# Performance work log

Measured on AMD Instinct MI355X. Metric: run time of the kernel, lower is better.

## Reference

```python
import jax, jax.numpy as jnp
import numpy as np
from jax import lax

BS, NV, CTX = 16, 7, 1536
PLEN, STRIDE = 16, 8
PN = (CTX - PLEN) // STRIDE + 1 + 1  # 192: end replication-pad adds one patch
D, H, DFF, L, TW = 512, 8, 2048, 3, 336
DK = D // H
SCALE = DK ** -0.5  # lsa=False -> fixed scale
NF = D * PN


def setup_inputs() -> dict:
    key = jax.random.key(0)
    ks = iter(jax.random.split(key, 40))

    def p(*shape, s=0.02):
        return jax.random.normal(next(ks), shape, jnp.float32) * s

    z = jax.random.normal(next(ks), (BS, NV, CTX), jnp.float32)
    # simpowerlaw decay mask: -|t|^scale, causal (-inf for k>q), one copy per layer
    t = np.arange(PN)
    times = t[:, None] - t[None, :]
    m = -np.abs(times).astype(np.float32) ** 0.25
    m[times < 0] = -np.inf
    decay_mask = jnp.asarray(np.broadcast_to(m, (L, PN, PN)).copy())
    return dict(
        z=z,
        W_P=p(PLEN, D), b_P=jnp.zeros((D,), jnp.float32),
        W_pos=p(PN, D),
        Wq=p(L, D, D), bq=jnp.zeros((L, D), jnp.float32),
        Wk=p(L, D, D), bk=jnp.zeros((L, D), jnp.float32),
        Wv=p(L, D, D), bv=jnp.zeros((L, D), jnp.float32),
        Wo=p(L, D, D), bo=jnp.zeros((L, D), jnp.float32),
        ln1_g=jnp.ones((L, D), jnp.float32), ln1_b=jnp.zeros((L, D), jnp.float32),
        W1=p(L, D, DFF), b1=jnp.zeros((L, DFF), jnp.float32),
        W2=p(L, DFF, D), b2=jnp.zeros((L, D), jnp.float32),
        ln2_g=jnp.ones((L, D), jnp.float32), ln2_b=jnp.zeros((L, D), jnp.float32),
        W_head=p(NF, TW, s=0.005), b_head=jnp.zeros((TW,), jnp.float32),
        decay_mask=decay_mask,
    )


def _ln(x, g, b):
    mu = x.mean(-1, keepdims=True)
    var = ((x - mu) ** 2).mean(-1, keepdims=True)
    return g * (x - mu) * lax.rsqrt(var + 1e-5) + b


def _forward(z, W_P, b_P, W_pos, Wq, bq, Wk, bk, Wv, bv, Wo, bo,
             ln1_g, ln1_b, W1, b1, W2, b2, ln2_g, ln2_b, W_head, b_head, decay_mask):
    bs, nv, _ = z.shape
    # replication pad end by STRIDE, then unfold into patches
    zp = jnp.concatenate([z, jnp.repeat(z[..., -1:], STRIDE, axis=-1)], axis=-1)
    idx = jnp.arange(PN)[:, None] * STRIDE + jnp.arange(PLEN)[None, :]
    patches = zp[..., idx]                      # [bs,nv,PN,PLEN]
    x = patches @ W_P + b_P                     # [bs,nv,PN,D]
    B = bs * nv
    src = x.reshape(B, PN, D) + W_pos           # channel-independent batch
    prev = jnp.zeros((B, H, PN, PN), src.dtype)  # residual attention carry

    def layer(carry, p):
        s, pr = carry
        wq, bq_, wk, bk_, wv, bv_, wo, bo_, g1, e1, w1, c1, w2, c2, g2, e2, dm = p
        q = (s @ wq + bq_).reshape(B, PN, H, DK).transpose(0, 2, 1, 3)
        k = (s @ wk + bk_).reshape(B, PN, H, DK).transpose(0, 2, 1, 3)
        v = (s @ wv + bv_).reshape(B, PN, H, DK).transpose(0, 2, 1, 3)
        scores = jnp.einsum('bhqd,bhkd->bhqk', q, k) * SCALE + pr + dm
        attn = jax.nn.softmax(scores, axis=-1)
        o = jnp.einsum('bhqk,bhkd->bhqd', attn, v).transpose(0, 2, 1, 3).reshape(B, PN, D)
        o = o @ wo + bo_
        s = _ln(s + o, g1, e1)                  # post-norm
        ff = jax.nn.gelu(s @ w1 + c1, approximate=False) @ w2 + c2
        s = _ln(s + ff, g2, e2)
        return (s, scores), None

    (src, _), _ = lax.scan(
        layer, (src, prev),
        (Wq, bq, Wk, bk, Wv, bv, Wo, bo, ln1_g, ln1_b, W1, b1, W2, b2, ln2_g, ln2_b, decay_mask))

    # Flatten_Head (individual=False): [bs,nv,D,PN] -> [bs,nv,D*PN] -> target_window
    xo = src.reshape(bs, nv, PN, D).transpose(0, 1, 3, 2).reshape(bs, nv, NF)
    return xo @ W_head + b_head                 # [bs,nv,TW]


def reference(z, W_P, b_P, W_pos, Wq, bq, Wk, bk, Wv, bv, Wo, bo,
              ln1_g, ln1_b, W1, b1, W2, b2, ln2_g, ln2_b, W_head, b_head, decay_mask):
    return _forward(z, W_P, b_P, W_pos, Wq, bq, Wk, bk, Wv, bv, Wo, bo,
                    ln1_g, ln1_b, W1, b1, W2, b2, ln2_g, ln2_b, W_head, b_head, decay_mask)
```

## Files before the change

kernel.cpp:

```cpp
#include <hip/hip_runtime.h>
#include <math.h>

#define BSZ 16
#define NV 7
#define CTX 1536
#define PN 192
#define PLEN 16
#define STRIDE 8
#define D 512
#define H 8
#define DK 64
#define DFF 2048
#define LYR 3
#define TW 336
#define NB 112
#define RTOT (NB * PN)
#define NF (D * PN)
#define SCALE 0.125f

typedef __attribute__((ext_vector_type(8))) short s16x8;
typedef __attribute__((ext_vector_type(4))) short s16x4;
typedef __attribute__((ext_vector_type(4))) float f32x4;

__device__ __forceinline__ unsigned short f2b(float f) {
  unsigned u = __builtin_bit_cast(unsigned, f);
  u = u + 0x7fffu + ((u >> 16) & 1u);
  return (unsigned short)(u >> 16);
}
__device__ __forceinline__ float b2f(unsigned short h) {
  unsigned u = ((unsigned)h) << 16;
  return __builtin_bit_cast(float, u);
}
__device__ __forceinline__ unsigned cvtpk(float lo, float hi) {
  unsigned r;
  asm("v_cvt_pk_bf16_f32 %0, %1, %2" : "=v"(r) : "v"(lo), "v"(hi));
  return r;
}
__device__ __forceinline__ float fast_exp2(float x) {
  float r; asm("v_exp_f32 %0, %1" : "=v"(r) : "v"(x)); return r;
}
__device__ __forceinline__ float fast_rcp(float x) {
  float r; asm("v_rcp_f32 %0, %1" : "=v"(r) : "v"(x)); return r;
}

__device__ __forceinline__ void glld(const unsigned short* g, short* l) {
  __builtin_amdgcn_global_load_lds(
      (const __attribute__((address_space(1))) void*)g,
      (__attribute__((address_space(3))) void*)l, 16, 0, 0);
}

__device__ __forceinline__ float gelu(float x) {
  float x2 = x * x;
  float u2 = x * fmaf(0.1029492f, x2, 2.3021186f);
  u2 = fminf(fmaxf(u2, -60.f), 60.f);
  float w = fast_exp2(u2);
  return x * w * fast_rcp(w + 1.0f);
}

__global__ __launch_bounds__(256) void k_patch_embed(
    const float* __restrict__ z, const float* __restrict__ W_P,
    const float* __restrict__ b_P, const float* __restrict__ W_pos,
    unsigned short* __restrict__ s) {
  int r = blockIdx.x;
  int bi = r / PN, p = r % PN;
  __shared__ float pv[PLEN];
  if (threadIdx.x < PLEN) {
    int t = p * STRIDE + threadIdx.x;
    pv[threadIdx.x] = z[(size_t)bi * CTX + (t < CTX ? t : CTX - 1)];
  }
  __syncthreads();
  for (int c = threadIdx.x; c < D; c += 256) {
    float acc = b_P[c] + W_pos[p * D + c];
#pragma unroll
    for (int j = 0; j < PLEN; j++) acc += pv[j] * W_P[j * D + c];
    s[(size_t)r * D + c] = f2b(acc);
  }
}

__global__ __launch_bounds__(256) void k_wtz(
    const float* __restrict__ W, unsigned short* __restrict__ Wt, int K, int N,
    size_t sstride, size_t dstride) {
  __shared__ float tile[32][33];
  const float* Wz = W + (size_t)blockIdx.z * sstride;
  unsigned short* Wtz = Wt + (size_t)blockIdx.z * dstride;
  int n0 = blockIdx.x * 32, k0 = blockIdx.y * 32;
  int tx = threadIdx.x & 31, ty = threadIdx.x >> 5;
#pragma unroll
  for (int i = 0; i < 4; i++)
    tile[ty + 8 * i][tx] =
        (n0 + tx < N) ? Wz[(size_t)(k0 + ty + 8 * i) * N + n0 + tx] : 0.0f;
  __syncthreads();
#pragma unroll
  for (int i = 0; i < 4; i++)
    if (n0 + ty + 8 * i < N)
      Wtz[(size_t)(n0 + ty + 8 * i) * K + k0 + tx] = f2b(tile[tx][ty + 8 * i]);
}

enum { EPI_QKV = 0, EPI_RES = 1, EPI_GELU = 2 };

template <int EPI, int N, int K>
__global__ __launch_bounds__(256) void k_mgemm(
    const unsigned short* __restrict__ Ap, const unsigned short* __restrict__ Wt,
    const float* __restrict__ bias0, const float* __restrict__ bias1,
    const float* __restrict__ bias2, const unsigned short* __restrict__ res,
    unsigned short* __restrict__ out0, unsigned short* __restrict__ out1,
    unsigned short* __restrict__ out2) {
  __shared__ short smem[24576];
  constexpr int NSTEP = K / 32;
  const int nx = N >> 7;
  const int nwg = gridDim.x;
  const int orig = blockIdx.x;
  const int wgid = (orig & 7) * (nwg >> 3) + (orig >> 3);
  const int m0 = (wgid / nx) * 128, n0 = (wgid % nx) * 128;
  const int t = threadIdx.x;
  const int w = t >> 6, l = t & 63;
  const int wr = (w >> 1) * 64, wc = (w & 1) * 64;
  const int lr = l & 15, lq = l >> 4;
  const int rsw = ((lr >> 1) & 3) << 3;
  const int srow = w * 32 + (l >> 2);
  const int scol = 8 * ((l & 3) ^ ((l >> 3) & 3));
  const unsigned short* gA = Ap + (size_t)(m0 + srow) * K + scol;
  const unsigned short* gB = Wt + (size_t)(n0 + srow) * K + scol;
  const int sbo = (w * 32) * 32;
  f32x4 acc[4][4] = {};

  auto STAGE = [&](int b, int kt) {
    short* dA = &smem[b * 8192 + sbo];
    short* dB = &smem[b * 8192 + 4096 + sbo];
    const int k0 = kt * 32;
    glld(gA + k0, dA);
    glld(gA + k0 + (size_t)16 * K, dA + 512);
    glld(gB + k0, dB);
    glld(gB + k0 + (size_t)16 * K, dB + 512);
  };

  STAGE(0, 0);
  STAGE(1, 1);
  int bc = 0, bs = 2;
  for (int step = 0; step < NSTEP; step++) {
    if (step + 2 < NSTEP) STAGE(bs, step + 2);
    if (step + 2 < NSTEP)      asm volatile("s_waitcnt vmcnt(8)" ::: "memory");
    else if (step + 1 < NSTEP) asm volatile("s_waitcnt vmcnt(4)" ::: "memory");
    else                       asm volatile("s_waitcnt vmcnt(0)" ::: "memory");
    __builtin_amdgcn_s_barrier();
    const short* cA = &smem[bc * 8192];
    const short* cB = &smem[bc * 8192 + 4096];
    s16x8 af[4], bf[4];
#pragma unroll
    for (int i = 0; i < 4; i++)
      af[i] = *(const s16x8*)&cA[(wr + i * 16 + lr) * 32 + ((lq * 8) ^ rsw)];
#pragma unroll
    for (int i = 0; i < 4; i++)
      bf[i] = *(const s16x8*)&cB[(wc + i * 16 + lr) * 32 + ((lq * 8) ^ rsw)];
#pragma unroll
    for (int i = 0; i < 4; i++)
#pragma unroll
      for (int j2 = 0; j2 < 4; j2++)
        acc[i][j2] = __builtin_amdgcn_mfma_f32_16x16x32_bf16(bf[j2], af[i], acc[i][j2], 0, 0, 0);
    asm volatile("s_waitcnt lgkmcnt(0)" ::: "memory");
    __builtin_amdgcn_s_barrier();
    bc++; if (bc == 3) bc = 0;
    bs++; if (bs == 3) bs = 0;
  }

  short* ot = smem;
  if (EPI == EPI_QKV) {
    const int which = n0 >> 9;
    const int ccb = n0 & 511;
    const float* bias = (which == 0) ? bias0 : (which == 1) ? bias1 : bias2;
    unsigned short* dst = (which == 0) ? out0 : (which == 1) ? out1 : out2;
    if (which < 2) {
#pragma unroll
      for (int i = 0; i < 4; i++) {
        const int ml = wr + i * 16 + lr;
#pragma unroll
        for (int j2 = 0; j2 < 4; j2++) {
          const int nl = wc + j2 * 16 + lq * 4;
          f32x4 a = acc[i][j2];
          float4 b4 = *(const float4*)&bias[ccb + nl];
          unsigned lo = cvtpk(a[0] + b4.x, a[1] + b4.y);
          unsigned hi = cvtpk(a[2] + b4.z, a[3] + b4.w);
          unsigned* d = (unsigned*)&ot[ml * 128 + ((nl >> 3) ^ (ml & 15)) * 8 + (nl & 7)];
          d[0] = lo; d[1] = hi;
        }
      }
      __syncthreads();
      const int r0 = t >> 1, cb = (t & 1) * 8;
      const int m = m0 + r0;
      const int bi2 = m / PN, p = m % PN;
#pragma unroll
      for (int q = 0; q < 8; q++) {
        int c = cb + q;
        int cc = ccb + c * 8;
        int hh = cc >> 6, dk8 = cc & 63;
        s16x8 vv = *(const s16x8*)&ot[r0 * 128 + ((c ^ (r0 & 15)) * 8)];
        *(s16x8*)&dst[(((size_t)bi2 * H + hh) * PN + p) * DK + dk8] = vv;
      }
    } else {
#pragma unroll
      for (int i = 0; i < 4; i++) {
        const int m = m0 + wr + i * 16 + lr;
        const int bi2 = m / PN, p = m % PN;
#pragma unroll
        for (int j2 = 0; j2 < 4; j2++) {
          const int nl = wc + j2 * 16 + lq * 4;
          f32x4 a = acc[i][j2];
#pragma unroll
          for (int r = 0; r < 4; r++) {
            int cc = ccb + nl + r;
            int hh = cc >> 6, dkk = cc & 63;
            dst[(((size_t)bi2 * H + hh) * DK + dkk) * PN + p] = f2b(a[r] + bias[cc]);
          }
        }
      }
    }
  } else {
#pragma unroll
    for (int i = 0; i < 4; i++) {
      const int ml = wr + i * 16 + lr;
#pragma unroll
      for (int j2 = 0; j2 < 4; j2++) {
        const int nl = wc + j2 * 16 + lq * 4;
        f32x4 a = acc[i][j2];
        float4 b4 = *(const float4*)&bias0[n0 + nl];
        float v0 = a[0] + b4.x, v1 = a[1] + b4.y;
        float v2 = a[2] + b4.z, v3 = a[3] + b4.w;
        if (EPI == EPI_GELU) {
          v0 = gelu(v0); v1 = gelu(v1); v2 = gelu(v2); v3 = gelu(v3);
        } else {
          s16x4 rr = *(const s16x4*)&res[(size_t)(m0 + ml) * N + n0 + nl];
          v0 += b2f((unsigned short)rr[0]); v1 += b2f((unsigned short)rr[1]);
          v2 += b2f((unsigned short)rr[2]); v3 += b2f((unsigned short)rr[3]);
        }
        unsigned lo = cvtpk(v0, v1), hi = cvtpk(v2, v3);
        unsigned* d = (unsigned*)&ot[ml * 128 + ((nl >> 3) ^ (ml & 15)) * 8 + (nl & 7)];
        d[0] = lo; d[1] = hi;
      }
    }
    __syncthreads();
    const int r0 = t >> 1, cb = (t & 1) * 8;
    const size_t orow = (size_t)(m0 + r0) * N + n0;
#pragma unroll
    for (int q = 0; q < 8; q++) {
      int c = cb + q;
      s16x8 vv = *(const s16x8*)&ot[r0 * 128 + ((c ^ (r0 & 15)) * 8)];
      *(s16x8*)&out0[orow + c * 8] = vv;
    }
  }
}

#define PSTR 196
template <int FIRST, int WRITEC>
__global__ __launch_bounds__(256) void k_attn(
    const unsigned short* __restrict__ qb, const unsigned short* __restrict__ kb,
    const unsigned short* __restrict__ vt, const float* __restrict__ dm,
    unsigned short* __restrict__ carry, unsigned short* __restrict__ ob) {
  __shared__ short Ps[96 * PSTR];
  __shared__ float redmax[2][96];
  __shared__ float redsum[2][96];
  int blk = blockIdx.x;
  int bh = blk >> 1, qh = blk & 1;
  int bi = bh >> 3, h = bh & 7;
  int t = threadIdx.x, w = t >> 6, l = t & 63;
  int wq = w >> 1, wk = w & 1;
  int lr = l & 15, lq = l >> 4, lk = lq * 8;
  const unsigned short* Q = qb + (size_t)bh * PN * DK + (size_t)qh * 96 * DK;
  const unsigned short* K = kb + (size_t)bh * PN * DK;
  f32x4 sv[3][6] = {};
#pragma unroll
  for (int ks = 0; ks < 2; ks++) {
    s16x8 af[3], bf[6];
#pragma unroll
    for (int i = 0; i < 3; i++)
      af[i] = *(const s16x8*)&Q[(size_t)(wq * 48 + i * 16 + lr) * DK + ks * 32 + lk];
#pragma unroll
    for (int j = 0; j < 6; j++)
      bf[j] = *(const s16x8*)&K[(size_t)(wk * 96 + j * 16 + lr) * DK + ks * 32 + lk];
#pragma unroll
    for (int i = 0; i < 3; i++)
#pragma unroll
      for (int j = 0; j < 6; j++)
        sv[i][j] = __builtin_amdgcn_mfma_f32_16x16x32_bf16(af[i], bf[j], sv[i][j], 0, 0, 0);
  }
  size_t cbase = (size_t)blk * 18432 + (size_t)(w * 18) * 256 + (size_t)l * 4;
#pragma unroll
  for (int i = 0; i < 3; i++) {
#pragma unroll
    for (int j = 0; j < 6; j++) {
      s16x4 cv;
      if (!FIRST) cv = *(const s16x4*)&carry[cbase + (i * 6 + j) * 256];
      s16x4 cw;
#pragma unroll
      for (int r = 0; r < 4; r++) {
        int row = qh * 96 + wq * 48 + i * 16 + lq * 4 + r;
        int col = wk * 96 + j * 16 + lr;
        float v = sv[i][j][r] * SCALE + dm[row * PN + col];
        if (!FIRST) v += b2f((unsigned short)cv[r]);
        if (WRITEC) cw[r] = (short)f2b(v);
        sv[i][j][r] = v;
      }
      if (WRITEC) *(s16x4*)&carry[cbase + (i * 6 + j) * 256] = cw;
    }
  }
#pragma unroll
  for (int i = 0; i < 3; i++) {
#pragma unroll
    for (int r = 0; r < 4; r++) {
      float m = sv[i][0][r];
#pragma unroll
      for (int j = 1; j < 6; j++) m = fmaxf(m, sv[i][j][r]);
#pragma unroll
      for (int off = 1; off < 16; off <<= 1) m = fmaxf(m, __shfl_xor(m, off));
      if (lr == 0) redmax[wk][wq * 48 + i * 16 + lq * 4 + r] = m;
    }
  }
  __syncthreads();
#pragma unroll
  for (int i = 0; i < 3; i++) {
#pragma unroll
    for (int r = 0; r < 4; r++) {
      int row = wq * 48 + i * 16 + lq * 4 + r;
      float fm = fmaxf(redmax[0][row], redmax[1][row]);
      float sum = 0.f;
#pragma unroll
      for (int j = 0; j < 6; j++) {
        float e = __expf(sv[i][j][r] - fm);
        sum += e;
        Ps[row * PSTR + wk * 96 + j * 16 + lr] = f2b(e);
      }
#pragma unroll
      for (int off = 1; off < 16; off <<= 1) sum += __shfl_xor(sum, off);
      if (lr == 0) redsum[wk][row] = sum;
    }
  }
  __syncthreads();
  const unsigned short* V = vt + (size_t)bh * DK * PN;
  f32x4 po[3][2] = {};
#pragma unroll
  for (int ks = 0; ks < 6; ks++) {
    s16x8 af[3], bf[2];
#pragma unroll
    for (int i = 0; i < 3; i++)
      af[i] = *(const s16x8*)&Ps[(wq * 48 + i * 16 + lr) * PSTR + ks * 32 + lk];
#pragma unroll
    for (int j = 0; j < 2; j++)
      bf[j] = *(const s16x8*)&V[(size_t)(wk * 32 + j * 16 + lr) * PN + ks * 32 + lk];
#pragma unroll
    for (int i = 0; i < 3; i++)
#pragma unroll
      for (int j = 0; j < 2; j++)
        po[i][j] = __builtin_amdgcn_mfma_f32_16x16x32_bf16(af[i], bf[j], po[i][j], 0, 0, 0);
  }
#pragma unroll
  for (int i = 0; i < 3; i++) {
#pragma unroll
    for (int r = 0; r < 4; r++) {
      int row = wq * 48 + i * 16 + lq * 4 + r;
      float inv = 1.0f / (redsum[0][row] + redsum[1][row]);
#pragma unroll
      for (int j = 0; j < 2; j++) {
        int dk = wk * 32 + j * 16 + lr;
        ob[((size_t)bi * PN + qh * 96 + row) * D + h * 64 + dk] = f2b(po[i][j][r] * inv);
      }
    }
  }
}

__global__ __launch_bounds__(256) void k_ln(
    const unsigned short* __restrict__ in, const float* __restrict__ g,
    const float* __restrict__ b, unsigned short* __restrict__ out) {
  int r = blockIdx.x * 4 + (threadIdx.x >> 6);
  int l = threadIdx.x & 63;
  const unsigned short* x = in + (size_t)r * D + l * 8;
  s16x8 xv = *(const s16x8*)x;
  float v[8], sm = 0.f, sq = 0.f;
#pragma unroll
  for (int j = 0; j < 8; j++) {
    v[j] = b2f((unsigned short)xv[j]);
    sm += v[j];
    sq += v[j] * v[j];
  }
#pragma unroll
  for (int off = 32; off > 0; off >>= 1) {
    sm += __shfl_xor(sm, off);
    sq += __shfl_xor(sq, off);
  }
  float mu = sm * (1.0f / D);
  float rs = rsqrtf(sq * (1.0f / D) - mu * mu + 1e-5f);
  float4 g0 = *(const float4*)&g[l * 8], g1 = *(const float4*)&g[l * 8 + 4];
  float4 b0 = *(const float4*)&b[l * 8], b1 = *(const float4*)&b[l * 8 + 4];
  float gg[8] = {g0.x, g0.y, g0.z, g0.w, g1.x, g1.y, g1.z, g1.w};
  float bb[8] = {b0.x, b0.y, b0.z, b0.w, b1.x, b1.y, b1.z, b1.w};
  s16x8 ov;
#pragma unroll
  for (int j = 0; j < 8; j++) ov[j] = (short)f2b(gg[j] * (v[j] - mu) * rs + bb[j]);
  *(s16x8*)(out + (size_t)r * D + l * 8) = ov;
}

__global__ __launch_bounds__(256) void k_transpose_b(
    const unsigned short* __restrict__ sb, unsigned short* __restrict__ xo) {
  __shared__ unsigned short tile[32][33];
  int d0 = blockIdx.x * 32, p0 = blockIdx.y * 32, bv = blockIdx.z;
  int tx = threadIdx.x & 31, ty = threadIdx.x >> 5;
#pragma unroll
  for (int i = 0; i < 4; i++)
    tile[ty + 8 * i][tx] = sb[((size_t)bv * PN + p0 + ty + 8 * i) * D + d0 + tx];
  __syncthreads();
#pragma unroll
  for (int i = 0; i < 4; i++)
    xo[(size_t)bv * NF + (size_t)(d0 + ty + 8 * i) * PN + p0 + tx] = tile[tx][ty + 8 * i];
}

__global__ __launch_bounds__(448) void k_head_mgemm(
    const unsigned short* __restrict__ A, const unsigned short* __restrict__ B,
    float* __restrict__ pp) {
  __shared__ short As[112 * 40];
  __shared__ short Bs[336 * 40];
  int kc = blockIdx.x;
  int t = threadIdx.x, w = t >> 6, l = t & 63;
  int lr = l & 15, lk = (l >> 4) * 8;
  int ar = t >> 2, ac = (t & 3) * 8;
  f32x4 acc[7][3] = {};
  for (int ks = 0; ks < 24; ks++) {
    int k0 = kc * 768 + ks * 32;
    s16x8 av = *(const s16x8*)&A[(size_t)ar * NF + k0 + ac];
    s16x8 bv0, bv1, bv2;
    {
      int i0 = t, i1 = t + 448, i2 = t + 896;
      bv0 = *(const s16x8*)&B[(size_t)(i0 >> 2) * NF + k0 + (i0 & 3) * 8];
      bv1 = *(const s16x8*)&B[(size_t)(i1 >> 2) * NF + k0 + (i1 & 3) * 8];
      bv2 = *(const s16x8*)&B[(size_t)(i2 >> 2) * NF + k0 + (i2 & 3) * 8];
    }
    __syncthreads();
    *(s16x8*)&As[ar * 40 + ac] = av;
    *(s16x8*)&Bs[(t >> 2) * 40 + (t & 3) * 8] = bv0;
    *(s16x8*)&Bs[((t + 448) >> 2) * 40 + (t & 3) * 8] = bv1;
    *(s16x8*)&Bs[((t + 896) >> 2) * 40 + (t & 3) * 8] = bv2;
    __syncthreads();
    s16x8 bf[3];
#pragma unroll
    for (int j = 0; j < 3; j++)
      bf[j] = *(const s16x8*)&Bs[((w * 3 + j) * 16 + lr) * 40 + lk];
#pragma unroll
    for (int mf = 0; mf < 7; mf++) {
      s16x8 af = *(const s16x8*)&As[(mf * 16 + lr) * 40 + lk];
#pragma unroll
      for (int j = 0; j < 3; j++)
        acc[mf][j] = __builtin_amdgcn_mfma_f32_16x16x32_bf16(af, bf[j], acc[mf][j], 0, 0, 0);
    }
  }
#pragma unroll
  for (int mf = 0; mf < 7; mf++) {
#pragma unroll
    for (int j = 0; j < 3; j++) {
#pragma unroll
      for (int r = 0; r < 4; r++) {
        int row = mf * 16 + (l >> 4) * 4 + r;
        int col = (w * 3 + j) * 16 + lr;
        pp[((size_t)kc * NB + row) * TW + col] = acc[mf][j][r];
      }
    }
  }
}

__global__ __launch_bounds__(256) void k_head_reduce(
    const float* __restrict__ pp, const float* __restrict__ bh,
    float* __restrict__ out) {
  int i = blockIdx.x * 256 + threadIdx.x;
  float s = bh[i % TW];
  for (int kc = 0; kc < 128; kc++) s += pp[(size_t)kc * (NB * TW) + i];
  out[i] = s;
}

extern "C" void kernel_launch(void* const* d_in, const int* in_sizes, int n_in,
                              void* d_out, int out_size, void* d_ws, size_t ws_size,
                              hipStream_t stream) {
  const float* z     = (const float*)d_in[0];
  const float* W_P   = (const float*)d_in[1];
  const float* b_P   = (const float*)d_in[2];
  const float* W_pos = (const float*)d_in[3];
  const float* Wq    = (const float*)d_in[4];
  const float* bq    = (const float*)d_in[5];
  const float* Wk    = (const float*)d_in[6];
  const float* bk    = (const float*)d_in[7];
  const float* Wv    = (const float*)d_in[8];
  const float* bv    = (const float*)d_in[9];
  const float* Wo    = (const float*)d_in[10];
  const float* bo    = (const float*)d_in[11];
  const float* ln1g  = (const float*)d_in[12];
  const float* ln1b  = (const float*)d_in[13];
  const float* W1    = (const float*)d_in[14];
  const float* b1    = (const float*)d_in[15];
  const float* W2    = (const float*)d_in[16];
  const float* b2    = (const float*)d_in[17];
  const float* ln2g  = (const float*)d_in[18];
  const float* ln2b  = (const float*)d_in[19];
  const float* Wh    = (const float*)d_in[20];
  const float* bh    = (const float*)d_in[21];
  const float* dmask = (const float*)d_in[22];
  float* out = (float*)d_out;

  char* ws = (char*)d_ws;
  unsigned short* s  = (unsigned short*)ws;
  unsigned short* sc = (unsigned short*)(ws + 22020096ull);
  unsigned short* qb = (unsigned short*)(ws + 88080384ull);
  unsigned short* kb = (unsigned short*)(ws + 110100480ull);
  unsigned short* vb = (unsigned short*)(ws + 132120576ull);
  unsigned short* ob = (unsigned short*)(ws + 154140672ull);
  unsigned short* tb = (unsigned short*)(ws + 176160768ull);
  unsigned short* hb = qb;
  unsigned short* t2 = tb;
  unsigned short* wt = (unsigned short*)(ws + 198180864ull);
  const size_t WLS = 3145728;
  unsigned short* xo  = (unsigned short*)(ws + 88080384ull);
  unsigned short* Wht = (unsigned short*)(ws + 110100480ull);
  float* pp = (float*)(ws + 22020096ull);

  k_patch_embed<<<RTOT, 256, 0, stream>>>(z, W_P, b_P, W_pos, s);

  k_wtz<<<dim3(16, 16, 3), 256, 0, stream>>>(Wq, wt + 0,       D, D,   262144, WLS);
  k_wtz<<<dim3(16, 16, 3), 256, 0, stream>>>(Wk, wt + 262144,  D, D,   262144, WLS);
  k_wtz<<<dim3(16, 16, 3), 256, 0, stream>>>(Wv, wt + 524288,  D, D,   262144, WLS);
  k_wtz<<<dim3(16, 16, 3), 256, 0, stream>>>(Wo, wt + 786432,  D, D,   262144, WLS);
  k_wtz<<<dim3(64, 16, 3), 256, 0, stream>>>(W1, wt + 1048576, D, DFF, 1048576, WLS);
  k_wtz<<<dim3(16, 64, 3), 256, 0, stream>>>(W2, wt + 2097152, DFF, D, 1048576, WLS);

  for (int l = 0; l < LYR; l++) {
    unsigned short* wtL = wt + (size_t)l * WLS;
    unsigned short* wqkv_t = wtL;
    unsigned short* wo_t   = wtL + 786432;
    unsigned short* w1_t   = wtL + 1048576;
    unsigned short* w2_t   = wtL + 2097152;

    k_mgemm<EPI_QKV, 1536, 512><<<2016, 256, 0, stream>>>(
        s, wqkv_t, bq + l * D, bk + l * D, bv + l * D, nullptr, qb, kb, vb);
    const float* dm = dmask + (size_t)l * PN * PN;
    if (l == 0)
      k_attn<1, 1><<<NB * H * 2, 256, 0, stream>>>(qb, kb, vb, dm, sc, ob);
    else if (l == LYR - 1)
      k_attn<0, 0><<<NB * H * 2, 256, 0, stream>>>(qb, kb, vb, dm, sc, ob);
    else
      k_attn<0, 1><<<NB * H * 2, 256, 0, stream>>>(qb, kb, vb, dm, sc, ob);
    k_mgemm<EPI_RES, 512, 512><<<672, 256, 0, stream>>>(
        ob, wo_t, bo + l * D, nullptr, nullptr, s, tb, nullptr, nullptr);
    k_ln<<<RTOT / 4, 256, 0, stream>>>(tb, ln1g + l * D, ln1b + l * D, s);
    k_mgemm<EPI_GELU, 2048, 512><<<2688, 256, 0, stream>>>(
        s, w1_t, b1 + l * DFF, nullptr, nullptr, nullptr, hb, nullptr, nullptr);
    k_mgemm<EPI_RES, 512, 2048><<<672, 256, 0, stream>>>(
        hb, w2_t, b2 + l * D, nullptr, nullptr, s, t2, nullptr, nullptr);
    k_ln<<<RTOT / 4, 256, 0, stream>>>(t2, ln2g + l * D, ln2b + l * D, s);
  }

  k_wtz<<<dim3(11, 3072, 1), 256, 0, stream>>>(Wh, Wht, NF, TW, 0, 0);
  k_transpose_b<<<dim3(16, 6, NB), 256, 0, stream>>>(s, xo);
  k_head_mgemm<<<128, 448, 0, stream>>>(xo, Wht, pp);
  k_head_reduce<<<147, 256, 0, stream>>>(pp, bh, out);
}
```

Baseline: 1.058 ms.

## Add 256x256-tile GEMM kernel for QKV and FFN1 projections

Introduces a second GEMM kernel with 512 threads, 256x256 output tiles, 64-wide K steps and double-buffered LDS staging, and uses it for the QKV and W1 GELU projections. The larger tile raises arithmetic intensity and cuts the number of workgroups and global reloads of A and W. It also remaps workgroup IDs across groups of eight to improve cache locality. The trade-off is heavier register pressure (128 accumulator floats per thread) and 128KB of LDS per block, which lowers occupancy, plus fewer blocks to balance across CUs.

After: 1.106 ms. +4.5%, slower.

```diff
diff --git a/kernel.cpp b/kernel.cpp
--- a/kernel.cpp
+++ b/kernel.cpp
@@ -164,57 +164,7 @@
   }
 
   short* ot = smem;
-  if (EPI == EPI_QKV) {
-    const int which = n0 >> 9;
-    const int ccb = n0 & 511;
-    const float* bias = (which == 0) ? bias0 : (which == 1) ? bias1 : bias2;
-    unsigned short* dst = (which == 0) ? out0 : (which == 1) ? out1 : out2;
-    if (which < 2) {
-#pragma unroll
-      for (int i = 0; i < 4; i++) {
-        const int ml = wr + i * 16 + lr;
-#pragma unroll
-        for (int j2 = 0; j2 < 4; j2++) {
-          const int nl = wc + j2 * 16 + lq * 4;
-          f32x4 a = acc[i][j2];
-          float4 b4 = *(const float4*)&bias[ccb + nl];
-          unsigned lo = cvtpk(a[0] + b4.x, a[1] + b4.y);
-          unsigned hi = cvtpk(a[2] + b4.z, a[3] + b4.w);
-          unsigned* d = (unsigned*)&ot[ml * 128 + ((nl >> 3) ^ (ml & 15)) * 8 + (nl & 7)];
-          d[0] = lo; d[1] = hi;
-        }
-      }
-      __syncthreads();
-      const int r0 = t >> 1, cb = (t & 1) * 8;
-      const int m = m0 + r0;
-      const int bi2 = m / PN, p = m % PN;
-#pragma unroll
-      for (int q = 0; q < 8; q++) {
-        int c = cb + q;
-        int cc = ccb + c * 8;
-        int hh = cc >> 6, dk8 = cc & 63;
-        s16x8 vv = *(const s16x8*)&ot[r0 * 128 + ((c ^ (r0 & 15)) * 8)];
-        *(s16x8*)&dst[(((size_t)bi2 * H + hh) * PN + p) * DK + dk8] = vv;
-      }
-    } else {
-#pragma unroll
-      for (int i = 0; i < 4; i++) {
-        const int m = m0 + wr + i * 16 + lr;
-        const int bi2 = m / PN, p = m % PN;
-#pragma unroll
-        for (int j2 = 0; j2 < 4; j2++) {
-          const int nl = wc + j2 * 16 + lq * 4;
-          f32x4 a = acc[i][j2];
-#pragma unroll
-          for (int r = 0; r < 4; r++) {
-            int cc = ccb + nl + r;
-            int hh = cc >> 6, dkk = cc & 63;
-            dst[(((size_t)bi2 * H + hh) * DK + dkk) * PN + p] = f2b(a[r] + bias[cc]);
-          }
-        }
-      }
-    }
-  } else {
+  {
 #pragma unroll
     for (int i = 0; i < 4; i++) {
       const int ml = wr + i * 16 + lr;
@@ -244,6 +194,154 @@
     for (int q = 0; q < 8; q++) {
       int c = cb + q;
       s16x8 vv = *(const s16x8*)&ot[r0 * 128 + ((c ^ (r0 & 15)) * 8)];
+      *(s16x8*)&out0[orow + c * 8] = vv;
+    }
+  }
+}
+
+template <int EPI, int N, int K>
+__global__ __launch_bounds__(512, 2) void k_mgemm2(
+    const unsigned short* __restrict__ Ap, const unsigned short* __restrict__ Wt,
+    const float* __restrict__ bias0, const float* __restrict__ bias1,
+    const float* __restrict__ bias2,
+    unsigned short* __restrict__ out0, unsigned short* __restrict__ out1,
+    unsigned short* __restrict__ out2) {
+  __shared__ short smem[65536];
+  constexpr int NSTEP = K / 64;
+  const int nx = N >> 8;
+  const int nwg = gridDim.x;
+  const int orig = blockIdx.x;
+  const int wgid = (orig & 7) * (nwg >> 3) + (orig >> 3);
+  const int m0 = (wgid / nx) * 256, n0 = (wgid % nx) * 256;
+  const int t = threadIdx.x;
+  const int w = t >> 6, l = t & 63;
+  const int wm = w >> 2, wn = w & 3;
+  const int lr = l & 15, lq = l >> 4;
+  const int srow = (w & 3) * 64 + (l >> 3);
+  const int scol = ((l & 7) ^ (l >> 3)) * 8;
+  const unsigned short* gsrc =
+      (w < 4) ? (Ap + (size_t)(m0 + srow) * K + scol)
+              : (Wt + (size_t)(n0 + srow) * K + scol);
+  short* sdst = &smem[(w >= 4 ? 16384 : 0) + (w & 3) * 4096];
+  f32x4 acc[8][4] = {};
+
+  auto STAGE = [&](int b, int kt) {
+    short* d = sdst + b * 32768;
+    const unsigned short* g = gsrc + kt * 64;
+#pragma unroll
+    for (int q = 0; q < 8; q++)
+      glld(g + (size_t)q * 8 * K, d + q * 512);
+  };
+
+  STAGE(0, 0);
+  for (int step = 0; step < NSTEP; step++) {
+    const int b = step & 1;
+    if (step + 1 < NSTEP) {
+      STAGE(b ^ 1, step + 1);
+      asm volatile("s_waitcnt vmcnt(8)" ::: "memory");
+    } else {
+      asm volatile("s_waitcnt vmcnt(0)" ::: "memory");
+    }
+    __builtin_amdgcn_s_barrier();
+    const short* cA = &smem[b * 32768];
+    const short* cB = &smem[b * 32768 + 16384];
+#pragma unroll
+    for (int kk = 0; kk < 2; kk++) {
+      s16x8 af[8], bf[4];
+#pragma unroll
+      for (int i = 0; i < 8; i++)
+        af[i] = *(const s16x8*)&cA[(wm * 128 + i * 16 + lr) * 64 +
+                                   (((kk * 4 + lq) ^ (lr & 7)) * 8)];
+#pragma unroll
+      for (int j = 0; j < 4; j++)
+        bf[j] = *(const s16x8*)&cB[(wn * 64 + j * 16 + lr) * 64 +
+                                   (((kk * 4 + lq) ^ (lr & 7)) * 8)];
+      __builtin_amdgcn_s_setprio(1);
+#pragma unroll
+      for (int i = 0; i < 8; i++)
+#pragma unroll
+        for (int j = 0; j < 4; j++)
+          acc[i][j] = __builtin_amdgcn_mfma_f32_16x16x32_bf16(bf[j], af[i], acc[i][j], 0, 0, 0);
+      __builtin_amdgcn_s_setprio(0);
+    }
+    asm volatile("s_waitcnt lgkmcnt(0)" ::: "memory");
+    __builtin_amdgcn_s_barrier();
+  }
+
+  short* ot = smem;
+  if (EPI == EPI_QKV) {
+    const int which = n0 >> 9;
+    const int ccb = n0 & 511;
+    const float* bias = (which == 0) ? bias0 : (which == 1) ? bias1 : bias2;
+    unsigned short* dst = (which == 0) ? out0 : (which == 1) ? out1 : out2;
+    if (which < 2) {
+#pragma unroll
+      for (int i = 0; i < 8; i++) {
+        const int ml = wm * 128 + i * 16 + lr;
+#pragma unroll
+        for (int j = 0; j < 4; j++) {
+          const int nl = wn * 64 + j * 16 + lq * 4;
+          f32x4 a = acc[i][j];
+          float4 b4 = *(const float4*)&bias[ccb + nl];
+          unsigned lo = cvtpk(a[0] + b4.x, a[1] + b4.y);
+          unsigned hi = cvtpk(a[2] + b4.z, a[3] + b4.w);
+          unsigned* d = (unsigned*)&ot[ml * 256 + ((nl >> 3) ^ (ml & 15)) * 8 + (nl & 7)];
+          d[0] = lo; d[1] = hi;
+        }
+      }
+      __syncthreads();
+      const int r0 = t >> 1, cb = (t & 1) * 16;
+      const int m = m0 + r0;
+      const int bi2 = m / PN, p = m % PN;
+#pragma unroll
+      for (int q = 0; q < 16; q++) {
+        int c = cb + q;
+        int cc = ccb + c * 8;
+        int hh = cc >> 6, dk8 = cc & 63;
+        s16x8 vv = *(const s16x8*)&ot[r0 * 256 + ((c ^ (r0 & 15)) * 8)];
+        *(s16x8*)&dst[(((size_t)bi2 * H + hh) * PN + p) * DK + dk8] = vv;
+      }
+    } else {
+#pragma unroll
+      for (int i = 0; i < 8; i++) {
+        const int m = m0 + wm * 128 + i * 16 + lr;
+        const int bi2 = m / PN, p = m % PN;
+#pragma unroll
+        for (int j = 0; j < 4; j++) {
+          const int nl = wn * 64 + j * 16 + lq * 4;
+          f32x4 a = acc[i][j];
+#pragma unroll
+          for (int r = 0; r < 4; r++) {
+            int cc = ccb + nl + r;
+            int hh = cc >> 6, dkk = cc & 63;
+            dst[(((size_t)bi2 * H + hh) * DK + dkk) * PN + p] = f2b(a[r] + bias[cc]);
+          }
+        }
+      }
+    }
+  } else {
+#pragma unroll
+    for (int i = 0; i < 8; i++) {
+      const int ml = wm * 128 + i * 16 + lr;
+#pragma unroll
+      for (int j = 0; j < 4; j++) {
+        const int nl = wn * 64 + j * 16 + lq * 4;
+        f32x4 a = acc[i][j];
+        float4 b4 = *(const float4*)&bias0[n0 + nl];
+        float v0 = gelu(a[0] + b4.x), v1 = gelu(a[1] + b4.y);
+        float v2 = gelu(a[2] + b4.z), v3 = gelu(a[3] + b4.w);
+        unsigned lo = cvtpk(v0, v1), hi = cvtpk(v2, v3);
+        unsigned* d = (unsigned*)&ot[ml * 256 + ((nl >> 3) ^ (ml & 15)) * 8 + (nl & 7)];
+        d[0] = lo; d[1] = hi;
+      }
+    }
+    __syncthreads();
+    const int r0 = t >> 1, cb = (t & 1) * 16;
+    const size_t orow = (size_t)(m0 + r0) * N + n0;
+#pragma unroll
+    for (int q = 0; q < 16; q++) {
+      int c = cb + q;
+      s16x8 vv = *(const s16x8*)&ot[r0 * 256 + ((c ^ (r0 & 15)) * 8)];
       *(s16x8*)&out0[orow + c * 8] = vv;
     }
   }
@@ -532,8 +630,8 @@
     unsigned short* w1_t   = wtL + 1048576;
     unsigned short* w2_t   = wtL + 2097152;
 
-    k_mgemm<EPI_QKV, 1536, 512><<<2016, 256, 0, stream>>>(
-        s, wqkv_t, bq + l * D, bk + l * D, bv + l * D, nullptr, qb, kb, vb);
+    k_mgemm2<EPI_QKV, 1536, 512><<<504, 512, 0, stream>>>(
+        s, wqkv_t, bq + l * D, bk + l * D, bv + l * D, qb, kb, vb);
     const float* dm = dmask + (size_t)l * PN * PN;
     if (l == 0)
       k_attn<1, 1><<<NB * H * 2, 256, 0, stream>>>(qb, kb, vb, dm, sc, ob);
@@ -544,8 +642,8 @@
     k_mgemm<EPI_RES, 512, 512><<<672, 256, 0, stream>>>(
         ob, wo_t, bo + l * D, nullptr, nullptr, s, tb, nullptr, nullptr);
     k_ln<<<RTOT / 4, 256, 0, stream>>>(tb, ln1g + l * D, ln1b + l * D, s);
-    k_mgemm<EPI_GELU, 2048, 512><<<2688, 256, 0, stream>>>(
-        s, w1_t, b1 + l * DFF, nullptr, nullptr, nullptr, hb, nullptr, nullptr);
+    k_mgemm2<EPI_GELU, 2048, 512><<<672, 512, 0, stream>>>(
+        s, w1_t, b1 + l * DFF, nullptr, nullptr, hb, nullptr, nullptr);
     k_mgemm<EPI_RES, 512, 2048><<<672, 256, 0, stream>>>(
         hb, w2_t, b2 + l * D, nullptr, nullptr, s, t2, nullptr, nullptr);
     k_ln<<<RTOT / 4, 256, 0, stream>>>(t2, ln2g + l * D, ln2b + l * D, s);
```
